# Optimization experiments

Hardware: AMD Instinct MI355X
Metric: run time of the kernel (lower is better)

The kernel has to match this reference:

```python
import jax, jax.numpy as jnp
import numpy as np
import math

V = 32000; SMAX = 256; N = 512; M = 16; TICKS = 4; D = 512
NSA = 256; NSO = 512; H = 8; HD = D // H; B = 2; S = 256


def _ln(x, g, b, eps=1e-5):
    m = x.mean(-1, keepdims=True)
    v = ((x - m) ** 2).mean(-1, keepdims=True)
    return (x - m) / jnp.sqrt(v + eps) * g + b


def _glu(x):
    a, b = jnp.split(x, 2, axis=-1)
    return a * jax.nn.sigmoid(b)


def setup_inputs() -> dict:
    key = jax.random.key(0)
    ks = iter(jax.random.split(key, 64))
    rn = lambda shape, s: jax.random.normal(next(ks), shape, jnp.float32) * s
    inp = {}
    inp['x'] = jax.random.randint(next(ks), (B, S), 0, V)
    inp['tok_table'] = rn((V, D), 0.02)
    inp['pos_embed'] = rn((SMAX, D), 0.02)
    inp['ln_emb_g'] = jnp.ones(D); inp['ln_emb_b'] = jnp.zeros(D)
    inp['kv_w'] = rn((D, D), 1 / math.sqrt(D)); inp['kv_b'] = jnp.zeros(D)
    inp['kv_ln_g'] = jnp.ones(D); inp['kv_ln_b'] = jnp.zeros(D)
    inp['q_w'] = rn((NSA, D), 1 / math.sqrt(NSA)); inp['q_b'] = jnp.zeros(D)
    inp['wq'] = rn((D, D), 1 / math.sqrt(D)); inp['bq'] = jnp.zeros(D)
    inp['wk'] = rn((D, D), 1 / math.sqrt(D)); inp['bk'] = jnp.zeros(D)
    inp['wv'] = rn((D, D), 1 / math.sqrt(D)); inp['bv'] = jnp.zeros(D)
    inp['ow'] = rn((D, D), 1 / math.sqrt(D)); inp['ob'] = jnp.zeros(D)
    inp['syn_w'] = rn((D + N, 2 * N), 1 / math.sqrt(D + N)); inp['syn_b'] = jnp.zeros(2 * N)
    inp['syn_g'] = jnp.ones(N); inp['syn_beta'] = jnp.zeros(N)
    inp['fc1_w'] = rn((N, M, 256), math.sqrt(2.0 / M)); inp['fc1_b'] = jnp.zeros((N, 256))
    inp['fc2_w'] = rn((N, 128, 2), math.sqrt(2.0 / 128)); inp['fc2_b'] = jnp.zeros((N, 2))
    inp['nlm_T'] = jnp.ones(1)
    a = math.sqrt(1.0 / N)
    inp['start_act'] = jax.random.uniform(next(ks), (SMAX, N), jnp.float32, -a, a)
    b2 = math.sqrt(1.0 / (N + M))
    inp['start_trace'] = jax.random.uniform(next(ks), (SMAX, N, M), jnp.float32, -b2, b2)
    inp['decay_a'] = jnp.zeros(NSA); inp['decay_o'] = jnp.zeros(NSO)
    inp['out_w'] = rn((NSO, V), 1 / math.sqrt(NSO)); inp['out_b'] = jnp.zeros(V)
    inp['idx_al'] = jax.random.randint(next(ks), (NSA,), 0, N)
    inp['idx_ar'] = jax.random.randint(next(ks), (NSA,), 0, N)
    inp['idx_ol'] = jax.random.randint(next(ks), (NSO,), 0, N)
    inp['idx_or'] = jax.random.randint(next(ks), (NSO,), 0, N)
    return inp


def reference(x, tok_table, pos_embed, ln_emb_g, ln_emb_b, kv_w, kv_b, kv_ln_g, kv_ln_b,
              q_w, q_b, wq, bq, wk, bk, wv, bv, ow, ob, syn_w, syn_b, syn_g, syn_beta,
              fc1_w, fc1_b, fc2_w, fc2_b, nlm_T, start_act, start_trace, decay_a, decay_o,
              out_w, out_b, idx_al, idx_ar, idx_ol, idx_or):
    Bz, Sl = x.shape
    emb = _ln(tok_table[x] + pos_embed[:Sl], ln_emb_g, ln_emb_b)        # (B,S,D)
    kv = _ln(emb @ kv_w + kv_b, kv_ln_g, kv_ln_b)
    k = (kv @ wk + bk).reshape(Bz, Sl, H, HD)                            # keys/values fixed over ticks
    v = (kv @ wv + bv).reshape(Bz, Sl, H, HD)
    mask = jnp.triu(jnp.ones((Sl, Sl), bool), 1)                         # True = masked
    r_a = jnp.exp(-decay_a)
    r_o = jnp.exp(-decay_o)
    act = jnp.broadcast_to(start_act[:Sl], (Bz, Sl, N))
    trace = jnp.broadcast_to(start_trace[:Sl], (Bz, Sl, N, M))
    aa = ba = ao_ = bo = None
    preds, certs = [], []
    for _ in range(TICKS):
        # action synchronization (decayed pairwise product)
        pp = act[:, :, idx_al] * act[:, :, idx_ar]
        if aa is None:
            aa, ba = pp, jnp.ones_like(pp)
        else:
            aa, ba = r_a * aa + pp, r_a * ba + 1.0
        sync_a = aa / jnp.sqrt(ba + 1e-8)
        # causal attention with query from action sync
        qh = ((sync_a @ q_w + q_b) @ wq + bq).reshape(Bz, Sl, H, HD)
        sc = jnp.einsum('bqhd,bkhd->bhqk', qh, k) / math.sqrt(HD)
        sc = jnp.where(mask, -1e9, sc)
        attn_out = jnp.einsum('bhqk,bkhd->bqhd', jax.nn.softmax(sc, -1), v).reshape(Bz, Sl, D) @ ow + ob
        # synapse MLP -> new pre-activation, shift memory trace
        state = _ln(_glu(jnp.concatenate([attn_out, act], -1) @ syn_w + syn_b), syn_g, syn_beta)
        trace = jnp.concatenate([trace[..., 1:], state[..., None]], -1)
        # per-neuron NLM (batched private GEMMs)
        h = _glu(jnp.einsum('bsnm,nmh->bsnh', trace, fc1_w) + fc1_b)
        o = _glu(jnp.einsum('bsnh,nho->bsno', h, fc2_w) + fc2_b)
        act = o[..., 0] / nlm_T[0]
        # output synchronization + prediction
        ppo = act[:, :, idx_ol] * act[:, :, idx_or]
        if ao_ is None:
            ao_, bo = ppo, jnp.ones_like(ppo)
        else:
            ao_, bo = r_o * ao_ + ppo, r_o * bo + 1.0
        pred = (ao_ / jnp.sqrt(bo + 1e-8)) @ out_w + out_b                # (B,S,V)
        p = jax.nn.softmax(pred, -1)
        ent = -(p * jnp.log(p + 1e-10)).sum(-1) / math.log(V)
        preds.append(pred)
        certs.append(jnp.stack([ent, 1.0 - ent], -1))
    return jnp.stack(preds, -1), jnp.stack(certs, -1)
```

## Files before the change

kernel.cpp:

```cpp
#include <hip/hip_runtime.h>
#include <cstdint>
#include <cstddef>

#define BATCH 2
#define SEQ   256
#define DIM   512
#define NN    512
#define MM    16
#define NTICK 4
#define NSA   256
#define NSO   512
#define NHEAD 8
#define HDIM  64
#define VOCAB 32000
#define BS    (BATCH*SEQ)
#define NBLK  500

typedef __bf16 bf16;
typedef bf16  bf16x4  __attribute__((ext_vector_type(4)));
typedef bf16  bf16x8v __attribute__((ext_vector_type(8)));
typedef float f32x4   __attribute__((ext_vector_type(4)));

typedef __attribute__((address_space(1))) const void av1_t;
typedef __attribute__((address_space(3))) void av3_t;

__global__ __launch_bounds__(256) void emb_ln_kernel(const int* __restrict__ x,
    const float* __restrict__ tok, const float* __restrict__ pos,
    const float* __restrict__ g, const float* __restrict__ b, float* __restrict__ out){
  int row = blockIdx.x, tid = threadIdx.x;
  int s = row & (SEQ-1);
  int token = x[row];
  const float* tr = tok + (size_t)token*DIM;
  const float* pr = pos + (size_t)s*DIM;
  float v0 = tr[tid]     + pr[tid];
  float v1 = tr[tid+256] + pr[tid+256];
  float sm = v0+v1, ss = v0*v0+v1*v1;
  #pragma unroll
  for (int o = 32; o > 0; o >>= 1){ sm += __shfl_down(sm, o); ss += __shfl_down(ss, o); }
  __shared__ float rs[4], rss[4];
  __shared__ float smean, sinv;
  int wid = tid >> 6, lane = tid & 63;
  if (lane == 0){ rs[wid] = sm; rss[wid] = ss; }
  __syncthreads();
  if (tid == 0){
    float S = rs[0]+rs[1]+rs[2]+rs[3];
    float SS = rss[0]+rss[1]+rss[2]+rss[3];
    float m = S * (1.0f/512.0f);
    float var = SS * (1.0f/512.0f) - m*m;
    smean = m; sinv = 1.0f/sqrtf(var + 1e-5f);
  }
  __syncthreads();
  float m = smean, inv = sinv;
  out[(size_t)row*512 + tid]       = (v0-m)*inv*g[tid]     + b[tid];
  out[(size_t)row*512 + tid + 256] = (v1-m)*inv*g[tid+256] + b[tid+256];
}

__global__ __launch_bounds__(256) void ln512_kernel(const float* __restrict__ in,
    const float* __restrict__ g, const float* __restrict__ b, float* __restrict__ out){
  int row = blockIdx.x, tid = threadIdx.x;
  const float* xr = in + (size_t)row*512;
  float v0 = xr[tid], v1 = xr[tid+256];
  float s = v0+v1, ss = v0*v0+v1*v1;
  #pragma unroll
  for (int o = 32; o > 0; o >>= 1){ s += __shfl_down(s, o); ss += __shfl_down(ss, o); }
  __shared__ float rs[4], rss[4];
  __shared__ float smean, sinv;
  int wid = tid >> 6, lane = tid & 63;
  if (lane == 0){ rs[wid] = s; rss[wid] = ss; }
  __syncthreads();
  if (tid == 0){
    float S = rs[0]+rs[1]+rs[2]+rs[3];
    float SS = rss[0]+rss[1]+rss[2]+rss[3];
    float m = S * (1.0f/512.0f);
    float var = SS * (1.0f/512.0f) - m*m;
    smean = m; sinv = 1.0f/sqrtf(var + 1e-5f);
  }
  __syncthreads();
  float m = smean, inv = sinv;
  out[(size_t)row*512 + tid]       = (v0-m)*inv*g[tid]     + b[tid];
  out[(size_t)row*512 + tid + 256] = (v1-m)*inv*g[tid+256] + b[tid+256];
}

__global__ __launch_bounds__(256) void glu_ln_kernel(const float* __restrict__ y,
    const float* __restrict__ g, const float* __restrict__ beta, float* __restrict__ out){
  int row = blockIdx.x, tid = threadIdx.x;
  const float* yr = y + (size_t)row*1024;
  float a0 = yr[tid],     b0 = yr[tid+512];
  float a1 = yr[tid+256], b1 = yr[tid+768];
  float g0 = a0 / (1.0f + expf(-b0));
  float g1 = a1 / (1.0f + expf(-b1));
  float s = g0+g1, ss = g0*g0+g1*g1;
  #pragma unroll
  for (int o = 32; o > 0; o >>= 1){ s += __shfl_down(s, o); ss += __shfl_down(ss, o); }
  __shared__ float rs[4], rss[4];
  __shared__ float smean, sinv;
  int wid = tid >> 6, lane = tid & 63;
  if (lane == 0){ rs[wid] = s; rss[wid] = ss; }
  __syncthreads();
  if (tid == 0){
    float S = rs[0]+rs[1]+rs[2]+rs[3];
    float SS = rss[0]+rss[1]+rss[2]+rss[3];
    float m = S * (1.0f/512.0f);
    float var = SS * (1.0f/512.0f) - m*m;
    smean = m; sinv = 1.0f/sqrtf(var + 1e-5f);
  }
  __syncthreads();
  float m = smean, inv = sinv;
  out[(size_t)row*512 + tid]       = (g0-m)*inv*g[tid]     + beta[tid];
  out[(size_t)row*512 + tid + 256] = (g1-m)*inv*g[tid+256] + beta[tid+256];
}

__global__ __launch_bounds__(256) void sync_kernel(const float* __restrict__ act,
    const int* __restrict__ il, const int* __restrict__ ir, const float* __restrict__ decay,
    float* __restrict__ accA, float* __restrict__ accB,
    float* __restrict__ outf, bf16* __restrict__ outb, int NS, int first){
  int i = blockIdx.x*256 + threadIdx.x;
  if (i >= BS*NS) return;
  int bs = i / NS, c = i - bs*NS;
  const float* ar = act + (size_t)bs*NN;
  float p = ar[il[c]] * ar[ir[c]];
  float A, Bv;
  if (first){ A = p; Bv = 1.0f; }
  else {
    float r = expf(-decay[c]);
    A = r*accA[i] + p;
    Bv = r*accB[i] + 1.0f;
  }
  accA[i] = A; accB[i] = Bv;
  float sy = A / sqrtf(Bv + 1e-8f);
  if (outf) outf[i] = sy;
  if (outb) outb[i] = (bf16)sy;
}

__global__ __launch_bounds__(256) void split_t(const float* __restrict__ W,
    bf16* __restrict__ hiT, bf16* __restrict__ loT, int K, int N){
  __shared__ float t[32][33];
  int n0 = blockIdx.x*32, k0 = blockIdx.y*32;
  int tid = threadIdx.x;
  int r = tid >> 3, c4 = (tid & 7)*4;
  float4 v = *(const float4*)(W + (size_t)(k0+r)*N + n0 + c4);
  t[r][c4+0]=v.x; t[r][c4+1]=v.y; t[r][c4+2]=v.z; t[r][c4+3]=v.w;
  __syncthreads();
  bf16x4 hi, lo;
  #pragma unroll
  for (int j = 0; j < 4; j++){
    float a = t[c4+j][r];
    bf16 h = (bf16)a;
    hi[j] = h;
    lo[j] = (bf16)(a - (float)h);
  }
  *(bf16x4*)(hiT + (size_t)(n0+r)*K + k0 + c4) = hi;
  if (loT) *(bf16x4*)(loT + (size_t)(n0+r)*K + k0 + c4) = lo;
}

__global__ __launch_bounds__(64) void gemm_x3(
    const float* __restrict__ A, const bf16* __restrict__ WhT,
    const bf16* __restrict__ WlT, const float* __restrict__ bias,
    float* __restrict__ C, int K, int lda, int ldc){
  int n0 = blockIdx.x * 64, m0 = blockIdx.y * 16;
  int lane = threadIdx.x;
  int ln = lane & 15, kq = lane >> 4;
  f32x4 acc[4];
  #pragma unroll
  for (int nf = 0; nf < 4; nf++) acc[nf] = (f32x4){0.f,0.f,0.f,0.f};
  const float* arow = A + (size_t)(m0 + ln)*lda + kq*8;
  const bf16* w0h = WhT + (size_t)(n0 + ln)*K + kq*8;
  const bf16* w0l = WlT + (size_t)(n0 + ln)*K + kq*8;
  size_t nstep = (size_t)16*K;
  for (int k0 = 0; k0 < K; k0 += 32){
    float4 a0 = *(const float4*)(arow + k0);
    float4 a1 = *(const float4*)(arow + k0 + 4);
    float av[8] = {a0.x,a0.y,a0.z,a0.w,a1.x,a1.y,a1.z,a1.w};
    bf16x8v ahi, alo;
    #pragma unroll
    for (int j = 0; j < 8; j++){
      bf16 h = (bf16)av[j];
      ahi[j] = h;
      alo[j] = (bf16)(av[j] - (float)h);
    }
    #pragma unroll
    for (int nf = 0; nf < 4; nf++){
      bf16x8v bh = *(const bf16x8v*)(w0h + nf*nstep + k0);
      bf16x8v bl = *(const bf16x8v*)(w0l + nf*nstep + k0);
      acc[nf] = __builtin_amdgcn_mfma_f32_16x16x32_bf16(ahi, bh, acc[nf], 0,0,0);
      acc[nf] = __builtin_amdgcn_mfma_f32_16x16x32_bf16(alo, bh, acc[nf], 0,0,0);
      acc[nf] = __builtin_amdgcn_mfma_f32_16x16x32_bf16(ahi, bl, acc[nf], 0,0,0);
    }
  }
  #pragma unroll
  for (int nf = 0; nf < 4; nf++){
    int col = n0 + nf*16 + ln;
    float bb = bias ? bias[col] : 0.0f;
    #pragma unroll
    for (int r = 0; r < 4; r++)
      C[(size_t)(m0 + kq*4 + r)*ldc + col] = acc[nf][r] + bb;
  }
}

__global__ void qbc_kernel(const float* __restrict__ qb, const float* __restrict__ wq,
                           const float* __restrict__ bq, float* __restrict__ qbc){
  int j = blockIdx.x*64 + threadIdx.x;
  float s = bq[j];
  for (int k = 0; k < DIM; k++) s = fmaf(qb[k], wq[(size_t)k*DIM + j], s);
  qbc[j] = s;
}

__global__ __launch_bounds__(256) void attn_kernel(const float* __restrict__ qh,
    const float* __restrict__ kb, const float* __restrict__ vb, float* __restrict__ outb){
  int qt = blockIdx.x, h = blockIdx.y, b = blockIdx.z;
  __shared__ float qs[16][HDIM];
  __shared__ float sc[16][SEQ + 4];
  __shared__ float red[16][16];
  __shared__ float rowm[16], rowz[16];
  int tid = threadIdx.x;
  {
    int r = tid >> 4, c4 = tid & 15;
    *(float4*)&qs[r][c4*4] =
      *(const float4*)(qh + ((size_t)(b*SEQ + qt*16 + r))*DIM + h*HDIM + c4*4);
  }
  __syncthreads();
  {
    int kk = tid;
    const float* krow = kb + ((size_t)(b*SEQ + kk))*DIM + h*HDIM;
    float s[16] = {};
    for (int d4 = 0; d4 < HDIM/4; d4++){
      float4 k4 = *(const float4*)(krow + d4*4);
      #pragma unroll
      for (int q = 0; q < 16; q++){
        float4 q4 = *(const float4*)&qs[q][d4*4];
        s[q] += q4.x*k4.x + q4.y*k4.y + q4.z*k4.z + q4.w*k4.w;
      }
    }
    #pragma unroll
    for (int q = 0; q < 16; q++){
      int qg = qt*16 + q;
      sc[q][kk] = (kk > qg) ? -1e9f : s[q]*0.125f;
    }
  }
  __syncthreads();
  {
    int q = tid >> 4, seg = tid & 15;
    float m = -1e30f;
    for (int i = 0; i < 16; i++) m = fmaxf(m, sc[q][seg*16+i]);
    red[q][seg] = m;
  }
  __syncthreads();
  if (tid < 16){
    float m = red[tid][0];
    for (int i = 1; i < 16; i++) m = fmaxf(m, red[tid][i]);
    rowm[tid] = m;
  }
  __syncthreads();
  {
    int q = tid >> 4, seg = tid & 15;
    float m = rowm[q], z = 0.0f;
    for (int i = 0; i < 16; i++){
      float e = expf(sc[q][seg*16+i] - m);
      sc[q][seg*16+i] = e;
      z += e;
    }
    red[q][seg] = z;
  }
  __syncthreads();
  if (tid < 16){
    float z = 0.0f;
    for (int i = 0; i < 16; i++) z += red[tid][i];
    rowz[tid] = 1.0f / z;
  }
  __syncthreads();
  {
    int q = tid >> 4, dc = tid & 15;
    float inv = rowz[q];
    float ax=0, ay=0, az=0, aw=0;
    for (int kk = 0; kk < SEQ; kk++){
      float p = sc[q][kk];
      float4 v4 = *(const float4*)(vb + ((size_t)(b*SEQ + kk))*DIM + h*HDIM + dc*4);
      ax = fmaf(p, v4.x, ax); ay = fmaf(p, v4.y, ay);
      az = fmaf(p, v4.z, az); aw = fmaf(p, v4.w, aw);
    }
    float4 o; o.x=ax*inv; o.y=ay*inv; o.z=az*inv; o.w=aw*inv;
    *(float4*)(outb + ((size_t)(b*SEQ + qt*16 + q))*DIM + h*HDIM + dc*4) = o;
  }
}

__global__ void act_init_kernel(const float* __restrict__ sa, float* __restrict__ act,
                                float* __restrict__ catb){
  int i = blockIdx.x*256 + threadIdx.x;
  float v = sa[i & (SEQ*NN - 1)];
  act[i] = v;
  int bs = i >> 9, n = i & 511;
  catb[(size_t)bs*1024 + 512 + n] = v;
}

__global__ __launch_bounds__(256) void nlm_kernel(
    const float* __restrict__ start_trace,
    const float* __restrict__ s0, const float* __restrict__ s1,
    const float* __restrict__ s2, const float* __restrict__ s3,
    const float* __restrict__ fc1w, const float* __restrict__ fc1b,
    const float* __restrict__ fc2w, const float* __restrict__ fc2b,
    const float* __restrict__ nlmT, float* __restrict__ act,
    float* __restrict__ catb, int t){
  int n = blockIdx.x, b = blockIdx.y, s = threadIdx.x;
  int bs = b*SEQ + s;
  size_t sidx = (size_t)bs*NN + n;
  float tr[16];
  #pragma unroll
  for (int j = 0; j < 16; j++){
    int src = j + t + 1;
    if (src < 16){
      tr[j] = start_trace[((size_t)s*NN + n)*MM + src];
    } else {
      int k = src - 16;
      tr[j] = (k==0) ? s0[sidx] : (k==1) ? s1[sidx] : (k==2) ? s2[sidx] : s3[sidx];
    }
  }
  const float* w1 = fc1w + (size_t)n*16*256;
  const float* b1 = fc1b + (size_t)n*256;
  const float* w2 = fc2w + (size_t)n*256;
  float o0 = fc2b[n*2+0], o1 = fc2b[n*2+1];
  #pragma unroll 4
  for (int j = 0; j < 128; j++){
    float a  = b1[j];
    float bb = b1[j+128];
    #pragma unroll
    for (int m = 0; m < 16; m++){
      a  = fmaf(tr[m], w1[m*256 + j],       a);
      bb = fmaf(tr[m], w1[m*256 + j + 128], bb);
    }
    float gg = a / (1.0f + expf(-bb));
    o0 = fmaf(gg, w2[j*2+0], o0);
    o1 = fmaf(gg, w2[j*2+1], o1);
  }
  float o = o0 / (1.0f + expf(-o1));
  float outv = o / nlmT[0];
  act[sidx] = outv;
  catb[(size_t)bs*1024 + 512 + n] = outv;
}

__global__ __launch_bounds__(512, 4) void out_gemm4(
    const bf16* __restrict__ sy0, const bf16* __restrict__ sy1,
    const bf16* __restrict__ sy2, const bf16* __restrict__ sy3,
    const bf16* __restrict__ WoT, const float* __restrict__ bo,
    float* __restrict__ outp, float* __restrict__ pm,
    float* __restrict__ pz, float* __restrict__ ps){
  __shared__ bf16 Bs[64*512];
  int tid = threadIdx.x;
  int w = tid >> 6, lane = tid & 63;
  int ln = lane & 15, kq = lane >> 4;
  int n0 = blockIdx.x * 64;

  {
    const char* gp = (const char*)(WoT + (size_t)n0*512);
    char* lp = (char*)Bs;
    #pragma unroll
    for (int it = 0; it < 8; ++it){
      int ub = (w*8 + it) << 10;
      int b  = ub + lane*16;
      int src = b ^ (((b >> 10) & 7) << 4);
      __builtin_amdgcn_global_load_lds((av1_t*)(gp + src), (av3_t*)(lp + ub),
                                       16, 0, 0);
    }
  }
  __syncthreads();

  float bb[4];
  #pragma unroll
  for (int nf = 0; nf < 4; ++nf) bb[nf] = bo[n0 + nf*16 + ln];

  const size_t aoff = (size_t)ln*512 + (size_t)kq*8;
  const char* Bsc = (const char*)Bs;
  const int bbase = (ln << 10) + (kq << 4);
  const int sw = (ln & 7) << 4;
  const int selt = ln & 3, selr = (ln >> 2) & 3;

  for (int i = 0; i < 4; ++i){
    int m0 = w*16 + i*128;
    const bf16* pa0 = sy0 + (size_t)m0*512 + aoff;
    const bf16* pa1 = sy1 + (size_t)m0*512 + aoff;
    const bf16* pa2 = sy2 + (size_t)m0*512 + aoff;
    const bf16* pa3 = sy3 + (size_t)m0*512 + aoff;
    f32x4 acc[4][4];
    #pragma unroll
    for (int t = 0; t < 4; ++t)
      #pragma unroll
      for (int nf = 0; nf < 4; ++nf) acc[t][nf] = (f32x4){0.f,0.f,0.f,0.f};

    #pragma unroll
    for (int k0 = 0; k0 < 512; k0 += 32){
      bf16x8v a0 = *(const bf16x8v*)(pa0 + k0);
      bf16x8v a1 = *(const bf16x8v*)(pa1 + k0);
      bf16x8v a2 = *(const bf16x8v*)(pa2 + k0);
      bf16x8v a3 = *(const bf16x8v*)(pa3 + k0);
      int kb = bbase + k0*2;
      bf16x8v b0 = *(const bf16x8v*)(Bsc + ((kb           ) ^ sw));
      bf16x8v b1 = *(const bf16x8v*)(Bsc + ((kb + 16*1024) ^ sw));
      bf16x8v b2 = *(const bf16x8v*)(Bsc + ((kb + 32*1024) ^ sw));
      bf16x8v b3 = *(const bf16x8v*)(Bsc + ((kb + 48*1024) ^ sw));
      acc[0][0] = __builtin_amdgcn_mfma_f32_16x16x32_bf16(a0, b0, acc[0][0], 0,0,0);
      acc[1][0] = __builtin_amdgcn_mfma_f32_16x16x32_bf16(a1, b0, acc[1][0], 0,0,0);
      acc[2][0] = __builtin_amdgcn_mfma_f32_16x16x32_bf16(a2, b0, acc[2][0], 0,0,0);
      acc[3][0] = __builtin_amdgcn_mfma_f32_16x16x32_bf16(a3, b0, acc[3][0], 0,0,0);
      acc[0][1] = __builtin_amdgcn_mfma_f32_16x16x32_bf16(a0, b1, acc[0][1], 0,0,0);
      acc[1][1] = __builtin_amdgcn_mfma_f32_16x16x32_bf16(a1, b1, acc[1][1], 0,0,0);
      acc[2][1] = __builtin_amdgcn_mfma_f32_16x16x32_bf16(a2, b1, acc[2][1], 0,0,0);
      acc[3][1] = __builtin_amdgcn_mfma_f32_16x16x32_bf16(a3, b1, acc[3][1], 0,0,0);
      acc[0][2] = __builtin_amdgcn_mfma_f32_16x16x32_bf16(a0, b2, acc[0][2], 0,0,0);
      acc[1][2] = __builtin_amdgcn_mfma_f32_16x16x32_bf16(a1, b2, acc[1][2], 0,0,0);
      acc[2][2] = __builtin_amdgcn_mfma_f32_16x16x32_bf16(a2, b2, acc[2][2], 0,0,0);
      acc[3][2] = __builtin_amdgcn_mfma_f32_16x16x32_bf16(a3, b2, acc[3][2], 0,0,0);
      acc[0][3] = __builtin_amdgcn_mfma_f32_16x16x32_bf16(a0, b3, acc[0][3], 0,0,0);
      acc[1][3] = __builtin_amdgcn_mfma_f32_16x16x32_bf16(a1, b3, acc[1][3], 0,0,0);
      acc[2][3] = __builtin_amdgcn_mfma_f32_16x16x32_bf16(a2, b3, acc[2][3], 0,0,0);
      acc[3][3] = __builtin_amdgcn_mfma_f32_16x16x32_bf16(a3, b3, acc[3][3], 0,0,0);
    }

    #pragma unroll
    for (int t = 0; t < 4; ++t)
      #pragma unroll
      for (int nf = 0; nf < 4; ++nf)
        #pragma unroll
        for (int r = 0; r < 4; ++r) acc[t][nf][r] += bb[nf];

    #pragma unroll
    for (int r = 0; r < 4; ++r){
      size_t rowoff = (size_t)(m0 + kq*4 + r)*VOCAB;
      #pragma unroll
      for (int nf = 0; nf < 4; ++nf){
        float4 o;
        o.x = acc[0][nf][r]; o.y = acc[1][nf][r];
        o.z = acc[2][nf][r]; o.w = acc[3][nf][r];
        *(float4*)(outp + (rowoff + n0 + nf*16 + ln)*4) = o;
      }
    }

    float mv = 0.f, zv = 0.f, sv = 0.f;
    #pragma unroll
    for (int t = 0; t < 4; ++t){
      #pragma unroll
      for (int r = 0; r < 4; ++r){
        float m = fmaxf(fmaxf(acc[t][0][r], acc[t][1][r]),
                        fmaxf(acc[t][2][r], acc[t][3][r]));
        #pragma unroll
        for (int o2 = 1; o2 < 16; o2 <<= 1) m = fmaxf(m, __shfl_xor(m, o2));
        float z = 0.0f, s = 0.0f;
        #pragma unroll
        for (int nf = 0; nf < 4; ++nf){
          float v = acc[t][nf][r] - m;
          float e = expf(v);
          z += e; s += v*e;
        }
        #pragma unroll
        for (int o2 = 1; o2 < 16; o2 <<= 1){ z += __shfl_xor(z, o2); s += __shfl_xor(s, o2); }
        if (t == selt && r == selr){ mv = m; zv = z; sv = s; }
      }
    }
    size_t p = ((size_t)blockIdx.x*512 + (m0 + kq*4 + selr))*4 + selt;
    pm[p] = mv; pz[p] = zv; ps[p] = sv;
  }
}

__global__ __launch_bounds__(64) void ent_final(const float* __restrict__ pm,
    const float* __restrict__ pz, const float* __restrict__ ps, float* __restrict__ certs){
  int row = blockIdx.x >> 2, t = blockIdx.x & 3;
  const size_t base = (size_t)row*4 + t;
  int lane = threadIdx.x;
  float M = -1e30f, Z = 0.0f, S = 0.0f;
  for (int i = lane; i < NBLK; i += 64){
    size_t idx = base + (size_t)i*2048;
    float m2 = pm[idx], z2 = pz[idx], s2 = ps[idx];
    float Mn = fmaxf(M, m2);
    float e1 = expf(M - Mn), e2 = expf(m2 - Mn);
    S = (S + (M - Mn)*Z)*e1 + (s2 + (m2 - Mn)*z2)*e2;
    Z = Z*e1 + z2*e2;
    M = Mn;
  }
  #pragma unroll
  for (int o = 1; o < 64; o <<= 1){
    float m2 = __shfl_xor(M, o), z2 = __shfl_xor(Z, o), s2 = __shfl_xor(S, o);
    float Mn = fmaxf(M, m2);
    float e1 = expf(M - Mn), e2 = expf(m2 - Mn);
    S = (S + (M - Mn)*Z)*e1 + (s2 + (m2 - Mn)*z2)*e2;
    Z = Z*e1 + z2*e2;
    M = Mn;
  }
  if (lane == 0){
    float ent = (logf(Z) - S/Z) * (1.0f / logf((float)VOCAB));
    certs[((size_t)row*2 + 0)*4 + t] = ent;
    certs[((size_t)row*2 + 1)*4 + t] = 1.0f - ent;
  }
}

extern "C" void kernel_launch(void* const* d_in, const int* in_sizes, int n_in,
                              void* d_out, int out_size, void* d_ws, size_t ws_size,
                              hipStream_t stream){
  const int*   x        = (const int*)  d_in[0];
  const float* tok      = (const float*)d_in[1];
  const float* pos      = (const float*)d_in[2];
  const float* ln_emb_g = (const float*)d_in[3];
  const float* ln_emb_b = (const float*)d_in[4];
  const float* kv_w     = (const float*)d_in[5];
  const float* kv_b     = (const float*)d_in[6];
  const float* kv_ln_g  = (const float*)d_in[7];
  const float* kv_ln_b  = (const float*)d_in[8];
  const float* q_w      = (const float*)d_in[9];
  const float* q_b      = (const float*)d_in[10];
  const float* wq       = (const float*)d_in[11];
  const float* bq       = (const float*)d_in[12];
  const float* wk       = (const float*)d_in[13];
  const float* bk       = (const float*)d_in[14];
  const float* wv       = (const float*)d_in[15];
  const float* bv       = (const float*)d_in[16];
  const float* ow       = (const float*)d_in[17];
  const float* ob       = (const float*)d_in[18];
  const float* syn_w    = (const float*)d_in[19];
  const float* syn_b    = (const float*)d_in[20];
  const float* syn_g    = (const float*)d_in[21];
  const float* syn_beta = (const float*)d_in[22];
  const float* fc1_w    = (const float*)d_in[23];
  const float* fc1_b    = (const float*)d_in[24];
  const float* fc2_w    = (const float*)d_in[25];
  const float* fc2_b    = (const float*)d_in[26];
  const float* nlm_T    = (const float*)d_in[27];
  const float* start_act   = (const float*)d_in[28];
  const float* start_trace = (const float*)d_in[29];
  const float* decay_a  = (const float*)d_in[30];
  const float* decay_o  = (const float*)d_in[31];
  const float* out_w    = (const float*)d_in[32];
  const float* out_b    = (const float*)d_in[33];
  const int* idx_al = (const int*)d_in[34];
  const int* idx_ar = (const int*)d_in[35];
  const int* idx_ol = (const int*)d_in[36];
  const int* idx_or = (const int*)d_in[37];

  char* wp = (char*)d_ws;
  auto alloc = [&](size_t bytes) -> void* {
    void* p = (void*)wp;
    wp += (bytes + 255) & ~(size_t)255;
    return p;
  };
  float* qwc      = (float*)alloc((size_t)256*512*4);
  float* qbc      = (float*)alloc(512*4);
  float* emb      = (float*)alloc((size_t)BS*512*4);
  float* kvt      = (float*)alloc((size_t)BS*512*4);
  float* kvn      = (float*)alloc((size_t)BS*512*4);
  float* kbuf     = (float*)alloc((size_t)BS*512*4);
  float* vbuf     = (float*)alloc((size_t)BS*512*4);
  float* act      = (float*)alloc((size_t)BS*512*4);
  float* aaB      = (float*)alloc((size_t)BS*256*4);
  float* baB      = (float*)alloc((size_t)BS*256*4);
  float* aoB      = (float*)alloc((size_t)BS*512*4);
  float* boB      = (float*)alloc((size_t)BS*512*4);
  float* sync_a   = (float*)alloc((size_t)BS*256*4);
  float* qh       = (float*)alloc((size_t)BS*512*4);
  float* attn_raw = (float*)alloc((size_t)BS*512*4);
  float* catb     = (float*)alloc((size_t)BS*1024*4);
  float* syn_y    = (float*)alloc((size_t)BS*1024*4);
  float* states[NTICK];
  for (int t = 0; t < NTICK; t++) states[t] = (float*)alloc((size_t)BS*512*4);
  bf16* syob[NTICK];
  for (int t = 0; t < NTICK; t++) syob[t] = (bf16*)alloc((size_t)BS*512*2);
  bf16* kvT_h = (bf16*)alloc((size_t)512*512*2);
  bf16* kvT_l = (bf16*)alloc((size_t)512*512*2);
  bf16* wkT_h = (bf16*)alloc((size_t)512*512*2);
  bf16* wkT_l = (bf16*)alloc((size_t)512*512*2);
  bf16* wvT_h = (bf16*)alloc((size_t)512*512*2);
  bf16* wvT_l = (bf16*)alloc((size_t)512*512*2);
  bf16* owT_h = (bf16*)alloc((size_t)512*512*2);
  bf16* owT_l = (bf16*)alloc((size_t)512*512*2);
  bf16* wqT_h = (bf16*)alloc((size_t)512*512*2);
  bf16* wqT_l = (bf16*)alloc((size_t)512*512*2);
  bf16* synT_h = (bf16*)alloc((size_t)1024*1024*2);
  bf16* synT_l = (bf16*)alloc((size_t)1024*1024*2);
  bf16* qwcT_h = (bf16*)alloc((size_t)512*256*2);
  bf16* qwcT_l = (bf16*)alloc((size_t)512*256*2);
  bf16* WoT    = (bf16*)alloc((size_t)VOCAB*512*2);
  float* pm = (float*)alloc((size_t)NBLK*512*4*4);
  float* pz = (float*)alloc((size_t)NBLK*512*4*4);
  float* ps = (float*)alloc((size_t)NBLK*512*4*4);

  float* preds = (float*)d_out;
  float* certs = (float*)d_out + (size_t)BS*VOCAB*NTICK;

  split_t<<<dim3(16,16), 256, 0, stream>>>(kv_w,  kvT_h, kvT_l, 512, 512);
  split_t<<<dim3(16,16), 256, 0, stream>>>(wk,    wkT_h, wkT_l, 512, 512);
  split_t<<<dim3(16,16), 256, 0, stream>>>(wv,    wvT_h, wvT_l, 512, 512);
  split_t<<<dim3(16,16), 256, 0, stream>>>(ow,    owT_h, owT_l, 512, 512);
  split_t<<<dim3(16,16), 256, 0, stream>>>(wq,    wqT_h, wqT_l, 512, 512);
  split_t<<<dim3(32,32), 256, 0, stream>>>(syn_w, synT_h, synT_l, 1024, 1024);
  split_t<<<dim3(VOCAB/32,16), 256, 0, stream>>>(out_w, WoT, nullptr, 512, VOCAB);

  emb_ln_kernel<<<BS, 256, 0, stream>>>(x, tok, pos, ln_emb_g, ln_emb_b, emb);
  gemm_x3<<<dim3(8,32), 64, 0, stream>>>(emb, kvT_h, kvT_l, kv_b, kvt, 512, 512, 512);
  ln512_kernel<<<BS, 256, 0, stream>>>(kvt, kv_ln_g, kv_ln_b, kvn);
  gemm_x3<<<dim3(8,32), 64, 0, stream>>>(kvn, wkT_h, wkT_l, bk, kbuf, 512, 512, 512);
  gemm_x3<<<dim3(8,32), 64, 0, stream>>>(kvn, wvT_h, wvT_l, bv, vbuf, 512, 512, 512);
  gemm_x3<<<dim3(8,16), 64, 0, stream>>>(q_w, wqT_h, wqT_l, nullptr, qwc, 512, 512, 512);
  split_t<<<dim3(16,8), 256, 0, stream>>>(qwc, qwcT_h, qwcT_l, 256, 512);
  qbc_kernel<<<8, 64, 0, stream>>>(q_b, wq, bq, qbc);
  act_init_kernel<<<(BS*NN)/256, 256, 0, stream>>>(start_act, act, catb);

  for (int t = 0; t < NTICK; t++){
    sync_kernel<<<(BS*NSA)/256, 256, 0, stream>>>(act, idx_al, idx_ar, decay_a,
        aaB, baB, sync_a, nullptr, NSA, t==0);
    gemm_x3<<<dim3(8,32), 64, 0, stream>>>(sync_a, qwcT_h, qwcT_l, qbc, qh, 256, 256, 512);
    attn_kernel<<<dim3(16, NHEAD, BATCH), 256, 0, stream>>>(qh, kbuf, vbuf, attn_raw);
    gemm_x3<<<dim3(8,32), 64, 0, stream>>>(attn_raw, owT_h, owT_l, ob, catb, 512, 512, 1024);
    gemm_x3<<<dim3(16,32), 64, 0, stream>>>(catb, synT_h, synT_l, syn_b, syn_y, 1024, 1024, 1024);
    glu_ln_kernel<<<BS, 256, 0, stream>>>(syn_y, syn_g, syn_beta, states[t]);
    nlm_kernel<<<dim3(NN, BATCH), 256, 0, stream>>>(start_trace,
        states[0], states[1], states[2], states[3],
        fc1_w, fc1_b, fc2_w, fc2_b, nlm_T, act, catb, t);
    sync_kernel<<<(BS*NSO)/256, 256, 0, stream>>>(act, idx_ol, idx_or, decay_o,
        aoB, boB, nullptr, syob[t], NSO, t==0);
  }

  out_gemm4<<<dim3(NBLK), 512, 0, stream>>>(
      syob[0], syob[1], syob[2], syob[3], WoT, out_b, preds, pm, pz, ps);
  ent_final<<<BS*4, 64, 0, stream>>>(pm, pz, ps, certs);
}
```

Measured before the change: 1.678 ms.

## Switch output GEMM to 32x32x16 MFMA tiles with 4-wave blocks

Rewrites the output projection kernel to use 32x32x16 bf16 MFMA instructions instead of 16x16x32, with 256-thread blocks where each wave covers 128 rows. The B tile is pre-permuted into LDS so each lane loads its fragment with one contiguous vector read, replacing the XOR-swizzled addressing. The entropy partial reduction now uses 32-lane shuffles. Intended effect: fewer MFMA issues and LDS reads per flop. In exchange it raises per-wave accumulator register pressure and halves the threads per block.

```diff
diff --git a/kernel.cpp b/kernel.cpp
--- a/kernel.cpp
+++ b/kernel.cpp
@@ -20,6 +20,7 @@
 typedef bf16  bf16x4  __attribute__((ext_vector_type(4)));
 typedef bf16  bf16x8v __attribute__((ext_vector_type(8)));
 typedef float f32x4   __attribute__((ext_vector_type(4)));
+typedef float f32x16  __attribute__((ext_vector_type(16)));
 
 typedef __attribute__((address_space(1))) const void av1_t;
 typedef __attribute__((address_space(3))) void av3_t;
@@ -337,7 +338,7 @@
   catb[(size_t)bs*1024 + 512 + n] = outv;
 }
 
-__global__ __launch_bounds__(512, 4) void out_gemm4(
+__global__ __launch_bounds__(256, 2) void out_gemm5(
     const bf16* __restrict__ sy0, const bf16* __restrict__ sy1,
     const bf16* __restrict__ sy2, const bf16* __restrict__ sy3,
     const bf16* __restrict__ WoT, const float* __restrict__ bo,
@@ -346,116 +347,98 @@
   __shared__ bf16 Bs[64*512];
   int tid = threadIdx.x;
   int w = tid >> 6, lane = tid & 63;
-  int ln = lane & 15, kq = lane >> 4;
+  int r31 = lane & 31, hi = lane >> 5;
   int n0 = blockIdx.x * 64;
 
   {
     const char* gp = (const char*)(WoT + (size_t)n0*512);
     char* lp = (char*)Bs;
     #pragma unroll
-    for (int it = 0; it < 8; ++it){
-      int ub = (w*8 + it) << 10;
-      int b  = ub + lane*16;
-      int src = b ^ (((b >> 10) & 7) << 4);
+    for (int it = 0; it < 16; ++it){
+      int ub = (w*16 + it) << 10;
+      int q  = (ub >> 4) + lane;
+      int c  = q & 31, h = (q >> 5) & 1, ks = (q >> 6) & 31, nf = (q >> 11) & 1;
+      int src = (nf*32 + c)*1024 + ks*32 + h*16;
       __builtin_amdgcn_global_load_lds((av1_t*)(gp + src), (av3_t*)(lp + ub),
                                        16, 0, 0);
     }
   }
   __syncthreads();
 
-  float bb[4];
-  #pragma unroll
-  for (int nf = 0; nf < 4; ++nf) bb[nf] = bo[n0 + nf*16 + ln];
-
-  const size_t aoff = (size_t)ln*512 + (size_t)kq*8;
-  const char* Bsc = (const char*)Bs;
-  const int bbase = (ln << 10) + (kq << 4);
-  const int sw = (ln & 7) << 4;
-  const int selt = ln & 3, selr = (ln >> 2) & 3;
+  float bb0 = bo[n0 + r31], bb1 = bo[n0 + 32 + r31];
+  const bf16x8v* Bv = (const bf16x8v*)Bs;
 
   for (int i = 0; i < 4; ++i){
-    int m0 = w*16 + i*128;
-    const bf16* pa0 = sy0 + (size_t)m0*512 + aoff;
-    const bf16* pa1 = sy1 + (size_t)m0*512 + aoff;
-    const bf16* pa2 = sy2 + (size_t)m0*512 + aoff;
-    const bf16* pa3 = sy3 + (size_t)m0*512 + aoff;
-    f32x4 acc[4][4];
+    int m0 = w*128 + i*32;
+    const bf16* pa0 = sy0 + (size_t)(m0 + r31)*512 + hi*8;
+    const bf16* pa1 = sy1 + (size_t)(m0 + r31)*512 + hi*8;
+    const bf16* pa2 = sy2 + (size_t)(m0 + r31)*512 + hi*8;
+    const bf16* pa3 = sy3 + (size_t)(m0 + r31)*512 + hi*8;
+    f32x16 acc[2][4];
+    #pragma unroll
+    for (int nf = 0; nf < 2; ++nf)
+      #pragma unroll
+      for (int t = 0; t < 4; ++t)
+        acc[nf][t] = (f32x16){0.f,0.f,0.f,0.f,0.f,0.f,0.f,0.f,
+                              0.f,0.f,0.f,0.f,0.f,0.f,0.f,0.f};
+
+    #pragma unroll 4
+    for (int ks = 0; ks < 32; ++ks){
+      bf16x8v a0 = *(const bf16x8v*)(pa0 + ks*16);
+      bf16x8v a1 = *(const bf16x8v*)(pa1 + ks*16);
+      bf16x8v a2 = *(const bf16x8v*)(pa2 + ks*16);
+      bf16x8v a3 = *(const bf16x8v*)(pa3 + ks*16);
+      bf16x8v b0 = Bv[       ks*64 + lane];
+      bf16x8v b1 = Bv[2048 + ks*64 + lane];
+      acc[0][0] = __builtin_amdgcn_mfma_f32_32x32x16_bf16(a0, b0, acc[0][0], 0,0,0);
+      acc[0][1] = __builtin_amdgcn_mfma_f32_32x32x16_bf16(a1, b0, acc[0][1], 0,0,0);
+      acc[0][2] = __builtin_amdgcn_mfma_f32_32x32x16_bf16(a2, b0, acc[0][2], 0,0,0);
+      acc[0][3] = __builtin_amdgcn_mfma_f32_32x32x16_bf16(a3, b0, acc[0][3], 0,0,0);
+      acc[1][0] = __builtin_amdgcn_mfma_f32_32x32x16_bf16(a0, b1, acc[1][0], 0,0,0);
+      acc[1][1] = __builtin_amdgcn_mfma_f32_32x32x16_bf16(a1, b1, acc[1][1], 0,0,0);
+      acc[1][2] = __builtin_amdgcn_mfma_f32_32x32x16_bf16(a2, b1, acc[1][2], 0,0,0);
+      acc[1][3] = __builtin_amdgcn_mfma_f32_32x32x16_bf16(a3, b1, acc[1][3], 0,0,0);
+    }
+
     #pragma unroll
     for (int t = 0; t < 4; ++t)
       #pragma unroll
-      for (int nf = 0; nf < 4; ++nf) acc[t][nf] = (f32x4){0.f,0.f,0.f,0.f};
-
-    #pragma unroll
-    for (int k0 = 0; k0 < 512; k0 += 32){
-      bf16x8v a0 = *(const bf16x8v*)(pa0 + k0);
-      bf16x8v a1 = *(const bf16x8v*)(pa1 + k0);
-      bf16x8v a2 = *(const bf16x8v*)(pa2 + k0);
-      bf16x8v a3 = *(const bf16x8v*)(pa3 + k0);
-      int kb = bbase + k0*2;
-      bf16x8v b0 = *(const bf16x8v*)(Bsc + ((kb           ) ^ sw));
-      bf16x8v b1 = *(const bf16x8v*)(Bsc + ((kb + 16*1024) ^ sw));
-      bf16x8v b2 = *(const bf16x8v*)(Bsc + ((kb + 32*1024) ^ sw));
-      bf16x8v b3 = *(const bf16x8v*)(Bsc + ((kb + 48*1024) ^ sw));
-      acc[0][0] = __builtin_amdgcn_mfma_f32_16x16x32_bf16(a0, b0, acc[0][0], 0,0,0);
-      acc[1][0] = __builtin_amdgcn_mfma_f32_16x16x32_bf16(a1, b0, acc[1][0], 0,0,0);
-      acc[2][0] = __builtin_amdgcn_mfma_f32_16x16x32_bf16(a2, b0, acc[2][0], 0,0,0);
-      acc[3][0] = __builtin_amdgcn_mfma_f32_16x16x32_bf16(a3, b0, acc[3][0], 0,0,0);
-      acc[0][1] = __builtin_amdgcn_mfma_f32_16x16x32_bf16(a0, b1, acc[0][1], 0,0,0);
-      acc[1][1] = __builtin_amdgcn_mfma_f32_16x16x32_bf16(a1, b1, acc[1][1], 0,0,0);
-      acc[2][1] = __builtin_amdgcn_mfma_f32_16x16x32_bf16(a2, b1, acc[2][1], 0,0,0);
-      acc[3][1] = __builtin_amdgcn_mfma_f32_16x16x32_bf16(a3, b1, acc[3][1], 0,0,0);
-      acc[0][2] = __builtin_amdgcn_mfma_f32_16x16x32_bf16(a0, b2, acc[0][2], 0,0,0);
-      acc[1][2] = __builtin_amdgcn_mfma_f32_16x16x32_bf16(a1, b2, acc[1][2], 0,0,0);
-      acc[2][2] = __builtin_amdgcn_mfma_f32_16x16x32_bf16(a2, b2, acc[2][2], 0,0,0);
-      acc[3][2] = __builtin_amdgcn_mfma_f32_16x16x32_bf16(a3, b2, acc[3][2], 0,0,0);
-      acc[0][3] = __builtin_amdgcn_mfma_f32_16x16x32_bf16(a0, b3, acc[0][3], 0,0,0);
-      acc[1][3] = __builtin_amdgcn_mfma_f32_16x16x32_bf16(a1, b3, acc[1][3], 0,0,0);
-      acc[2][3] = __builtin_amdgcn_mfma_f32_16x16x32_bf16(a2, b3, acc[2][3], 0,0,0);
-      acc[3][3] = __builtin_amdgcn_mfma_f32_16x16x32_bf16(a3, b3, acc[3][3], 0,0,0);
-    }
-
-    #pragma unroll
-    for (int t = 0; t < 4; ++t)
-      #pragma unroll
-      for (int nf = 0; nf < 4; ++nf)
-        #pragma unroll
-        for (int r = 0; r < 4; ++r) acc[t][nf][r] += bb[nf];
-
-    #pragma unroll
-    for (int r = 0; r < 4; ++r){
-      size_t rowoff = (size_t)(m0 + kq*4 + r)*VOCAB;
-      #pragma unroll
-      for (int nf = 0; nf < 4; ++nf){
-        float4 o;
-        o.x = acc[0][nf][r]; o.y = acc[1][nf][r];
-        o.z = acc[2][nf][r]; o.w = acc[3][nf][r];
-        *(float4*)(outp + (rowoff + n0 + nf*16 + ln)*4) = o;
+      for (int r = 0; r < 16; ++r){
+        acc[0][t][r] += bb0;
+        acc[1][t][r] += bb1;
       }
-    }
-
-    float mv = 0.f, zv = 0.f, sv = 0.f;
+
+    #pragma unroll
+    for (int r = 0; r < 16; ++r){
+      int mloc = (r & 3) + 8*(r >> 2) + 4*hi;
+      size_t rowoff = (size_t)(m0 + mloc)*VOCAB;
+      float4 o0, o1;
+      o0.x = acc[0][0][r]; o0.y = acc[0][1][r]; o0.z = acc[0][2][r]; o0.w = acc[0][3][r];
+      o1.x = acc[1][0][r]; o1.y = acc[1][1][r]; o1.z = acc[1][2][r]; o1.w = acc[1][3][r];
+      *(float4*)(outp + (rowoff + n0 + r31)*4)      = o0;
+      *(float4*)(outp + (rowoff + n0 + 32 + r31)*4) = o1;
+    }
+
     #pragma unroll
     for (int t = 0; t < 4; ++t){
       #pragma unroll
-      for (int r = 0; r < 4; ++r){
-        float m = fmaxf(fmaxf(acc[t][0][r], acc[t][1][r]),
-                        fmaxf(acc[t][2][r], acc[t][3][r]));
+      for (int r = 0; r < 16; ++r){
+        float v0 = acc[0][t][r], v1 = acc[1][t][r];
+        float mx = fmaxf(v0, v1);
         #pragma unroll
-        for (int o2 = 1; o2 < 16; o2 <<= 1) m = fmaxf(m, __shfl_xor(m, o2));
-        float z = 0.0f, s = 0.0f;
+        for (int o2 = 1; o2 < 32; o2 <<= 1) mx = fmaxf(mx, __shfl_xor(mx, o2));
+        float d0 = v0 - mx, d1 = v1 - mx;
+        float e0 = expf(d0), e1 = expf(d1);
+        float z = e0 + e1, s = d0*e0 + d1*e1;
         #pragma unroll
-        for (int nf = 0; nf < 4; ++nf){
-          float v = acc[t][nf][r] - m;
-          float e = expf(v);
-          z += e; s += v*e;
+        for (int o2 = 1; o2 < 32; o2 <<= 1){ z += __shfl_xor(z, o2); s += __shfl_xor(s, o2); }
+        if (r31 == 0){
+          int mloc = (r & 3) + 8*(r >> 2) + 4*hi;
+          size_t p = ((size_t)blockIdx.x*512 + m0 + mloc)*4 + t;
+          pm[p] = mx; pz[p] = z; ps[p] = s;
         }
-        #pragma unroll
-        for (int o2 = 1; o2 < 16; o2 <<= 1){ z += __shfl_xor(z, o2); s += __shfl_xor(s, o2); }
-        if (t == selt && r == selr){ mv = m; zv = z; sv = s; }
       }
     }
-    size_t p = ((size_t)blockIdx.x*512 + (m0 + kq*4 + selr))*4 + selt;
-    pm[p] = mv; pz[p] = zv; ps[p] = sv;
   }
 }
 
@@ -614,7 +597,7 @@
         aoB, boB, nullptr, syob[t], NSO, t==0);
   }
 
-  out_gemm4<<<dim3(NBLK), 512, 0, stream>>>(
+  out_gemm5<<<dim3(NBLK), 256, 0, stream>>>(
       syob[0], syob[1], syob[2], syob[3], WoT, out_b, preds, pm, pz, ps);
   ent_final<<<BS*4, 64, 0, stream>>>(pm, pz, ps, certs);
 }
```

Measured after the change: 1.454 ms. -13.3%, faster.
